# Performance work log

Hardware: AMD Instinct MI355X
Metric: run time of the kernel (lower is better)

## Reference

```python
import jax, jax.numpy as jnp
import numpy as np

B = 1048576  # batch
N = 5        # number of parallel LSTMs
H = 2        # input_size == hidden_size
CLS = 24     # 5*H + 14 others
OUT = 5


def setup_inputs() -> dict:
    key = jax.random.key(0)
    ks = jax.random.split(key, 10)
    s = 0.1
    return {
        "seqs": jax.random.normal(ks[0], (N, 1, B, H), dtype=jnp.float32),
        "others": jax.random.normal(ks[1], (1, B, 14), dtype=jnp.float32),
        # stacked LSTM params (PyTorch layout: gates ordered i,f,g,o; 4H rows)
        "w_ih": jax.random.normal(ks[2], (N, 4 * H, H), dtype=jnp.float32) * s,
        "w_hh": jax.random.normal(ks[3], (N, 4 * H, H), dtype=jnp.float32) * s,  # unused for T=1, h0=0
        "b_ih": jax.random.normal(ks[4], (N, 4 * H), dtype=jnp.float32) * s,
        "b_hh": jax.random.normal(ks[5], (N, 4 * H), dtype=jnp.float32) * s,
        # classifier: Linear(24,24) -> ReLU -> Linear(24,5) -> Sigmoid (torch layout: y = x @ W.T + b)
        "w1": jax.random.normal(ks[6], (CLS, CLS), dtype=jnp.float32) * s,
        "b1": jax.random.normal(ks[7], (CLS,), dtype=jnp.float32) * s,
        "w2": jax.random.normal(ks[8], (OUT, CLS), dtype=jnp.float32) * s,
        "b2": jax.random.normal(ks[9], (OUT,), dtype=jnp.float32) * s,
    }


def reference(seqs, others, w_ih, w_hh, b_ih, b_hh, w1, b1, w2, b2):
    # Each LSTM sees a length-1 sequence with h0=c0=0, so the recurrent
    # matmul (w_hh @ h0) vanishes and a single fused step suffices.
    x = seqs[:, 0]                                    # [N, B, H]
    gates = jnp.einsum("nbh,ngh->nbg", x, w_ih) + (b_ih + b_hh)[:, None, :]  # [N, B, 4H]
    i, f, g, o = jnp.split(gates, 4, axis=-1)         # each [N, B, H]
    c = jax.nn.sigmoid(i) * jnp.tanh(g)               # f*c0 = 0
    h = jax.nn.sigmoid(o) * jnp.tanh(c)               # [N, B, H]
    # concat the 5 LSTM outputs (dim order 0..4) then 'others', along features
    feats = jnp.concatenate([h.transpose(1, 0, 2).reshape(B, N * H), others[0]], axis=-1)  # [B, 24]
    hidden = jax.nn.relu(feats @ w1.T + b1)           # [B, 24]
    return jax.nn.sigmoid(hidden @ w2.T + b2)         # [B, 5]
```

## Files before the change

### kernel.cpp

```cpp
#include <hip/hip_runtime.h>


constexpr int Bc = 1048576;
constexpr int Nc = 5;

typedef __attribute__((ext_vector_type(8))) short bf16x8;
typedef __attribute__((ext_vector_type(16))) float f32x16;

__device__ __forceinline__ unsigned cvtpk(float lo, float hi) {
    unsigned r;
    asm("v_cvt_pk_bf16_f32 %0, %1, %2" : "=v"(r) : "v"(lo), "v"(hi));
    return r;
}
__device__ __forceinline__ void swap32(unsigned &x, unsigned &y) {
    asm("v_permlane32_swap_b32 %0, %1" : "+v"(x), "+v"(y));
}
__device__ __forceinline__ float fast_sigmoid(float x) {
    return __builtin_amdgcn_rcpf(1.0f + __expf(-x));
}
__device__ __forceinline__ float sigtanh(float a, float b) {
    float ea = __expf(-a);
    float eb = __expf(2.0f * b);
    return (eb - 1.0f) * __builtin_amdgcn_rcpf((eb + 1.0f) * (1.0f + ea));
}
__device__ __forceinline__ bf16x8 mk_frag(unsigned a, unsigned b,
                                          unsigned c, unsigned d) {
    union { uint4 u; bf16x8 v; } x;
    x.u = make_uint4(a, b, c, d);
    return x.v;
}
__device__ __forceinline__ bf16x8 pack_row8(const float* row, bool valid) {
    unsigned h0 = 0, h1 = 0, h2 = 0, h3 = 0;
    if (valid) {
        float4 a = *reinterpret_cast<const float4*>(row);
        float4 b = *reinterpret_cast<const float4*>(row + 4);
        h0 = cvtpk(a.x, a.y); h1 = cvtpk(a.z, a.w);
        h2 = cvtpk(b.x, b.y); h3 = cvtpk(b.z, b.w);
    }
    return mk_frag(h0, h1, h2, h3);
}

__global__ __launch_bounds__(256) void fused_rnn_mlp_v11(
    const float* __restrict__ seqs,
    const float* __restrict__ others,
    const float* __restrict__ w_ih,
    const float* __restrict__ b_ih,
    const float* __restrict__ b_hh,
    const float* __restrict__ w1,
    const float* __restrict__ b1,
    const float* __restrict__ w2,
    const float* __restrict__ b2,
    float* __restrict__ out)
{
    const int tid  = threadIdx.x;
    const int lane = tid & 63;
    const int lo31 = lane & 31;
    const int kh   = lane >> 5;
    const int base = blockIdx.x * 512;

    const bf16x8 A1a = pack_row8(w1 + lo31 * 24 + 8 * kh, lo31 < 24);
    const bf16x8 A1b = pack_row8(w1 + lo31 * 24 + 16, (lo31 < 24) && (kh == 0));
    const bf16x8 A2a = pack_row8(w2 + lo31 * 24 + 8 * kh, lo31 < 5);
    const bf16x8 A2b = pack_row8(w2 + lo31 * 24 + 16, (lo31 < 5) && (kh == 0));

    f32x16 c1z;
#pragma unroll
    for (int r = 0; r < 16; r++) {
        const int jb = (r & 3) + 8 * (r >> 2);
        float v = 0.0f;
        if (jb < 24) v = kh ? b1[jb + 4] : b1[jb];
        c1z[r] = v;
    }

#pragma unroll
    for (int g = 0; g < 2; g++) {
        const int elem  = base + g * 256 + tid;
        const int wbase = base + g * 256 + (tid >> 6) * 64;

        float2 x[Nc];
#pragma unroll
        for (int n = 0; n < Nc; n++)
            x[n] = *reinterpret_cast<const float2*>(
                seqs + ((size_t)n * Bc + elem) * 2);
        float2 oth[7];
        {
            const float2* op =
                reinterpret_cast<const float2*>(others + (size_t)elem * 14);
#pragma unroll
            for (int j = 0; j < 7; j++) oth[j] = op[j];
        }

        unsigned d[12];
#pragma unroll
        for (int n = 0; n < Nc; n++) {
            const float* w = w_ih + n * 16;
            const float bi0 = b_ih[n*8+0] + b_hh[n*8+0];
            const float bi1 = b_ih[n*8+1] + b_hh[n*8+1];
            const float bg0 = b_ih[n*8+4] + b_hh[n*8+4];
            const float bg1 = b_ih[n*8+5] + b_hh[n*8+5];
            const float bo0 = b_ih[n*8+6] + b_hh[n*8+6];
            const float bo1 = b_ih[n*8+7] + b_hh[n*8+7];
            float gi0 = fmaf(x[n].x, w[0],  fmaf(x[n].y, w[1],  bi0));
            float gi1 = fmaf(x[n].x, w[2],  fmaf(x[n].y, w[3],  bi1));
            float gg0 = fmaf(x[n].x, w[8],  fmaf(x[n].y, w[9],  bg0));
            float gg1 = fmaf(x[n].x, w[10], fmaf(x[n].y, w[11], bg1));
            float go0 = fmaf(x[n].x, w[12], fmaf(x[n].y, w[13], bo0));
            float go1 = fmaf(x[n].x, w[14], fmaf(x[n].y, w[15], bo1));
            float c0 = sigtanh(gi0, gg0);
            float c1 = sigtanh(gi1, gg1);
            d[n] = cvtpk(sigtanh(go0, c0), sigtanh(go1, c1));
        }
#pragma unroll
        for (int j = 0; j < 7; j++)
            d[5 + j] = cvtpk(oth[j].x, oth[j].y);

        unsigned b0a[4], b1a[4], b0b[4], b1b[4];
#pragma unroll
        for (int i = 0; i < 4; i++) {
            b0a[i] = d[i];     b1a[i] = d[4 + i];  swap32(b0a[i], b1a[i]);
            b0b[i] = d[8 + i]; b1b[i] = 0u;        swap32(b0b[i], b1b[i]);
        }

        f32x16 accA = c1z, accB = c1z;
        accA = __builtin_amdgcn_mfma_f32_32x32x16_bf16(
            A1a, mk_frag(b0a[0], b0a[1], b0a[2], b0a[3]), accA, 0, 0, 0);
        accA = __builtin_amdgcn_mfma_f32_32x32x16_bf16(
            A1b, mk_frag(b0b[0], b0b[1], b0b[2], b0b[3]), accA, 0, 0, 0);
        accB = __builtin_amdgcn_mfma_f32_32x32x16_bf16(
            A1a, mk_frag(b1a[0], b1a[1], b1a[2], b1a[3]), accB, 0, 0, 0);
        accB = __builtin_amdgcn_mfma_f32_32x32x16_bf16(
            A1b, mk_frag(b1b[0], b1b[1], b1b[2], b1b[3]), accB, 0, 0, 0);

#pragma unroll
        for (int t = 0; t < 2; t++) {
            const f32x16 acc = t ? accB : accA;
            unsigned p0 = cvtpk(fmaxf(acc[0],  0.f), fmaxf(acc[1],  0.f));
            unsigned p1 = cvtpk(fmaxf(acc[2],  0.f), fmaxf(acc[3],  0.f));
            unsigned p2 = cvtpk(fmaxf(acc[4],  0.f), fmaxf(acc[5],  0.f));
            unsigned p3 = cvtpk(fmaxf(acc[6],  0.f), fmaxf(acc[7],  0.f));
            unsigned p4 = cvtpk(fmaxf(acc[8],  0.f), fmaxf(acc[9],  0.f));
            unsigned p5 = cvtpk(fmaxf(acc[10], 0.f), fmaxf(acc[11], 0.f));
            unsigned w0 = p0, w2 = p2;  swap32(w0, w2);
            unsigned w1 = p1, w3 = p3;  swap32(w1, w3);
            unsigned u0 = p4, u2 = 0u;  swap32(u0, u2);
            unsigned u1 = p5, u3 = 0u;  swap32(u1, u3);
            const bf16x8 B2a = mk_frag(w0, w1, w2, w3);
            const bf16x8 B2b = mk_frag(u0, u1, u2, u3);

            f32x16 c2;
#pragma unroll
            for (int r = 0; r < 16; r++) c2[r] = 0.0f;
            c2[0] = kh ? b2[4] : b2[0];
            if (!kh) { c2[1] = b2[1]; c2[2] = b2[2]; c2[3] = b2[3]; }
            c2 = __builtin_amdgcn_mfma_f32_32x32x16_bf16(A2a, B2a, c2, 0, 0, 0);
            c2 = __builtin_amdgcn_mfma_f32_32x32x16_bf16(A2b, B2b, c2, 0, 0, 0);

            const float s0 = fast_sigmoid(c2[0]);
            const float s1 = fast_sigmoid(c2[1]);
            const float s2 = fast_sigmoid(c2[2]);
            const float s3 = fast_sigmoid(c2[3]);
            const int et = wbase + t * 32 + lo31;
            float* o = out + (size_t)et * 5;
            if (kh == 0) {
                o[0] = s0; o[1] = s1; o[2] = s2; o[3] = s3;
            } else {
                o[4] = s0;
            }
        }
    }
}

extern "C" void kernel_launch(void* const* d_in, const int* in_sizes, int n_in,
                              void* d_out, int out_size, void* d_ws, size_t ws_size,
                              hipStream_t stream) {
    const float* seqs   = (const float*)d_in[0];
    const float* others = (const float*)d_in[1];
    const float* w_ih   = (const float*)d_in[2];
    const float* b_ih   = (const float*)d_in[4];
    const float* b_hh   = (const float*)d_in[5];
    const float* w1     = (const float*)d_in[6];
    const float* b1     = (const float*)d_in[7];
    const float* w2     = (const float*)d_in[8];
    const float* b2     = (const float*)d_in[9];
    float* out = (float*)d_out;

    dim3 grid(Bc / 512), block(256);
    fused_rnn_mlp_v11<<<grid, block, 0, stream>>>(
        seqs, others, w_ih, b_ih, b_hh, w1, b1, w2, b2, out);
}
```

Before: 30.43 us.

## Convert to persistent grid-stride loop with register prefetch of next inputs

Launches a fixed grid of 1024 blocks that loop over 4 chunks of the batch, in place of 2048 blocks each handling two 256-element groups. Weight fragments and combined LSTM biases are set up once per block. Each iteration issues the loads for the next chunk before running the MFMA classifier, so memory latency overlaps compute. The first-layer MFMAs move into the per-half loop to lower register pressure. The cost is fewer blocks in flight, the extra registers held by the prefetched inputs, and a serial loop dependency.

```diff
diff --git a/kernel.cpp b/kernel.cpp
--- a/kernel.cpp
+++ b/kernel.cpp
@@ -1,8 +1,10 @@
 #include <hip/hip_runtime.h>
 
 
-constexpr int Bc = 1048576;
-constexpr int Nc = 5;
+constexpr int Bc    = 1048576;
+constexpr int Nc    = 5;
+constexpr int NBLK  = 1024;
+constexpr int NITER = Bc / (NBLK * 256);
 
 typedef __attribute__((ext_vector_type(8))) short bf16x8;
 typedef __attribute__((ext_vector_type(16))) float f32x16;
@@ -39,8 +41,18 @@
     }
     return mk_frag(h0, h1, h2, h3);
 }
+__device__ __forceinline__ void load_inputs(const float* __restrict__ seqs,
+                                            const float* __restrict__ others,
+                                            int e, float2 (&x)[Nc], float2 (&oth)[7]) {
+#pragma unroll
+    for (int n = 0; n < Nc; n++)
+        x[n] = *reinterpret_cast<const float2*>(seqs + ((size_t)n * Bc + e) * 2);
+    const float2* op = reinterpret_cast<const float2*>(others + (size_t)e * 14);
+#pragma unroll
+    for (int j = 0; j < 7; j++) oth[j] = op[j];
+}
 
-__global__ __launch_bounds__(256) void fused_rnn_mlp_v11(
+__global__ __launch_bounds__(256) void fused_rnn_mlp_v13(
     const float* __restrict__ seqs,
     const float* __restrict__ others,
     const float* __restrict__ w_ih,
@@ -56,7 +68,6 @@
     const int lane = tid & 63;
     const int lo31 = lane & 31;
     const int kh   = lane >> 5;
-    const int base = blockIdx.x * 512;
 
     const bf16x8 A1a = pack_row8(w1 + lo31 * 24 + 8 * kh, lo31 < 24);
     const bf16x8 A1b = pack_row8(w1 + lo31 * 24 + 16, (lo31 < 24) && (kh == 0));
@@ -71,41 +82,35 @@
         if (jb < 24) v = kh ? b1[jb + 4] : b1[jb];
         c1z[r] = v;
     }
+    float cb[6 * Nc];
+#pragma unroll
+    for (int n = 0; n < Nc; n++) {
+        cb[6*n+0] = b_ih[n*8+0] + b_hh[n*8+0];
+        cb[6*n+1] = b_ih[n*8+1] + b_hh[n*8+1];
+        cb[6*n+2] = b_ih[n*8+4] + b_hh[n*8+4];
+        cb[6*n+3] = b_ih[n*8+5] + b_hh[n*8+5];
+        cb[6*n+4] = b_ih[n*8+6] + b_hh[n*8+6];
+        cb[6*n+5] = b_ih[n*8+7] + b_hh[n*8+7];
+    }
 
-#pragma unroll
-    for (int g = 0; g < 2; g++) {
-        const int elem  = base + g * 256 + tid;
-        const int wbase = base + g * 256 + (tid >> 6) * 64;
+    float2 x[Nc], oth[7];
+    load_inputs(seqs, others, blockIdx.x * 256 + tid, x, oth);
 
-        float2 x[Nc];
-#pragma unroll
-        for (int n = 0; n < Nc; n++)
-            x[n] = *reinterpret_cast<const float2*>(
-                seqs + ((size_t)n * Bc + elem) * 2);
-        float2 oth[7];
-        {
-            const float2* op =
-                reinterpret_cast<const float2*>(others + (size_t)elem * 14);
-#pragma unroll
-            for (int j = 0; j < 7; j++) oth[j] = op[j];
-        }
+#pragma unroll 1
+    for (int k = 0; k < NITER; k++) {
+        const int cbase = (k * NBLK + blockIdx.x) * 256;
+        const int wbase = cbase + (tid >> 6) * 64;
 
         unsigned d[12];
 #pragma unroll
         for (int n = 0; n < Nc; n++) {
             const float* w = w_ih + n * 16;
-            const float bi0 = b_ih[n*8+0] + b_hh[n*8+0];
-            const float bi1 = b_ih[n*8+1] + b_hh[n*8+1];
-            const float bg0 = b_ih[n*8+4] + b_hh[n*8+4];
-            const float bg1 = b_ih[n*8+5] + b_hh[n*8+5];
-            const float bo0 = b_ih[n*8+6] + b_hh[n*8+6];
-            const float bo1 = b_ih[n*8+7] + b_hh[n*8+7];
-            float gi0 = fmaf(x[n].x, w[0],  fmaf(x[n].y, w[1],  bi0));
-            float gi1 = fmaf(x[n].x, w[2],  fmaf(x[n].y, w[3],  bi1));
-            float gg0 = fmaf(x[n].x, w[8],  fmaf(x[n].y, w[9],  bg0));
-            float gg1 = fmaf(x[n].x, w[10], fmaf(x[n].y, w[11], bg1));
-            float go0 = fmaf(x[n].x, w[12], fmaf(x[n].y, w[13], bo0));
-            float go1 = fmaf(x[n].x, w[14], fmaf(x[n].y, w[15], bo1));
+            float gi0 = fmaf(x[n].x, w[0],  fmaf(x[n].y, w[1],  cb[6*n+0]));
+            float gi1 = fmaf(x[n].x, w[2],  fmaf(x[n].y, w[3],  cb[6*n+1]));
+            float gg0 = fmaf(x[n].x, w[8],  fmaf(x[n].y, w[9],  cb[6*n+2]));
+            float gg1 = fmaf(x[n].x, w[10], fmaf(x[n].y, w[11], cb[6*n+3]));
+            float go0 = fmaf(x[n].x, w[12], fmaf(x[n].y, w[13], cb[6*n+4]));
+            float go1 = fmaf(x[n].x, w[14], fmaf(x[n].y, w[15], cb[6*n+5]));
             float c0 = sigtanh(gi0, gg0);
             float c1 = sigtanh(gi1, gg1);
             d[n] = cvtpk(sigtanh(go0, c0), sigtanh(go1, c1));
@@ -114,6 +119,10 @@
         for (int j = 0; j < 7; j++)
             d[5 + j] = cvtpk(oth[j].x, oth[j].y);
 
+        if (k + 1 < NITER)
+            load_inputs(seqs, others, ((k + 1) * NBLK + blockIdx.x) * 256 + tid,
+                        x, oth);
+
         unsigned b0a[4], b1a[4], b0b[4], b1b[4];
 #pragma unroll
         for (int i = 0; i < 4; i++) {
@@ -121,19 +130,18 @@
             b0b[i] = d[8 + i]; b1b[i] = 0u;        swap32(b0b[i], b1b[i]);
         }
 
-        f32x16 accA = c1z, accB = c1z;
-        accA = __builtin_amdgcn_mfma_f32_32x32x16_bf16(
-            A1a, mk_frag(b0a[0], b0a[1], b0a[2], b0a[3]), accA, 0, 0, 0);
-        accA = __builtin_amdgcn_mfma_f32_32x32x16_bf16(
-            A1b, mk_frag(b0b[0], b0b[1], b0b[2], b0b[3]), accA, 0, 0, 0);
-        accB = __builtin_amdgcn_mfma_f32_32x32x16_bf16(
-            A1a, mk_frag(b1a[0], b1a[1], b1a[2], b1a[3]), accB, 0, 0, 0);
-        accB = __builtin_amdgcn_mfma_f32_32x32x16_bf16(
-            A1b, mk_frag(b1b[0], b1b[1], b1b[2], b1b[3]), accB, 0, 0, 0);
-
 #pragma unroll
         for (int t = 0; t < 2; t++) {
-            const f32x16 acc = t ? accB : accA;
+            f32x16 acc = c1z;
+            acc = __builtin_amdgcn_mfma_f32_32x32x16_bf16(
+                A1a, mk_frag(t ? b1a[0] : b0a[0], t ? b1a[1] : b0a[1],
+                             t ? b1a[2] : b0a[2], t ? b1a[3] : b0a[3]),
+                acc, 0, 0, 0);
+            acc = __builtin_amdgcn_mfma_f32_32x32x16_bf16(
+                A1b, mk_frag(t ? b1b[0] : b0b[0], t ? b1b[1] : b0b[1],
+                             t ? b1b[2] : b0b[2], t ? b1b[3] : b0b[3]),
+                acc, 0, 0, 0);
+
             unsigned p0 = cvtpk(fmaxf(acc[0],  0.f), fmaxf(acc[1],  0.f));
             unsigned p1 = cvtpk(fmaxf(acc[2],  0.f), fmaxf(acc[3],  0.f));
             unsigned p2 = cvtpk(fmaxf(acc[4],  0.f), fmaxf(acc[5],  0.f));
@@ -141,19 +149,19 @@
             unsigned p4 = cvtpk(fmaxf(acc[8],  0.f), fmaxf(acc[9],  0.f));
             unsigned p5 = cvtpk(fmaxf(acc[10], 0.f), fmaxf(acc[11], 0.f));
             unsigned w0 = p0, w2 = p2;  swap32(w0, w2);
-            unsigned w1 = p1, w3 = p3;  swap32(w1, w3);
+            unsigned w1v = p1, w3 = p3; swap32(w1v, w3);
             unsigned u0 = p4, u2 = 0u;  swap32(u0, u2);
             unsigned u1 = p5, u3 = 0u;  swap32(u1, u3);
-            const bf16x8 B2a = mk_frag(w0, w1, w2, w3);
-            const bf16x8 B2b = mk_frag(u0, u1, u2, u3);
 
             f32x16 c2;
 #pragma unroll
             for (int r = 0; r < 16; r++) c2[r] = 0.0f;
             c2[0] = kh ? b2[4] : b2[0];
             if (!kh) { c2[1] = b2[1]; c2[2] = b2[2]; c2[3] = b2[3]; }
-            c2 = __builtin_amdgcn_mfma_f32_32x32x16_bf16(A2a, B2a, c2, 0, 0, 0);
-            c2 = __builtin_amdgcn_mfma_f32_32x32x16_bf16(A2b, B2b, c2, 0, 0, 0);
+            c2 = __builtin_amdgcn_mfma_f32_32x32x16_bf16(
+                A2a, mk_frag(w0, w1v, w2, w3), c2, 0, 0, 0);
+            c2 = __builtin_amdgcn_mfma_f32_32x32x16_bf16(
+                A2b, mk_frag(u0, u1, u2, u3), c2, 0, 0, 0);
 
             const float s0 = fast_sigmoid(c2[0]);
             const float s1 = fast_sigmoid(c2[1]);
@@ -184,7 +192,7 @@
     const float* b2     = (const float*)d_in[9];
     float* out = (float*)d_out;
 
-    dim3 grid(Bc / 512), block(256);
-    fused_rnn_mlp_v11<<<grid, block, 0, stream>>>(
+    dim3 grid(NBLK), block(256);
+    fused_rnn_mlp_v13<<<grid, block, 0, stream>>>(
         seqs, others, w_ih, b_ih, b_hh, w1, b1, w2, b2, out);
 }
```

Measured after the change: 31.57 us. +3.7%, slower.
